# Optimization experiments

Measured on AMD Instinct MI355X. Metric: run time of the kernel, lower is better.

Reference implementation:

```python
import jax, jax.numpy as jnp
import numpy as np

TEMPERATURE = 0.1
EPS = 1e-8  # torch F.cosine_similarity denom clamp


def setup_inputs() -> dict:
    key = jax.random.key(0)
    k1, k2, k3 = jax.random.split(key, 3)
    B, M, D, K = 8, 256, 768, 100
    N = B * M
    transformer_outputs = jax.random.normal(k1, (B, M, D), dtype=jnp.float32)
    cnn_targets = jax.random.normal(k2, (B, M, D), dtype=jnp.float32)
    # uniform sampling with replacement over [0, N) excluding self (multinomial on uniform mask)
    r = jax.random.randint(k3, (N, K), 0, N - 1)
    i = jnp.arange(N)[:, None]
    neg_indices = (r + (r >= i)).astype(jnp.int32)
    return {"transformer_outputs": transformer_outputs, "cnn_targets": cnn_targets, "neg_indices": neg_indices}


def reference(transformer_outputs, cnn_targets, neg_indices):
    B, M, D = transformer_outputs.shape
    N = B * M
    preds = transformer_outputs.reshape(N, D)
    targets = cnn_targets.reshape(N, D)
    pn = preds / jnp.clip(jnp.linalg.norm(preds, axis=-1, keepdims=True), EPS)
    tn = targets / jnp.clip(jnp.linalg.norm(targets, axis=-1, keepdims=True), EPS)
    # all pairwise cosine sims [N, N]; positive on the diagonal, negatives gathered by index
    sim = pn @ tn.T
    pos = jnp.diagonal(sim)                                   # [N]
    neg = sim[jnp.arange(N)[:, None], neg_indices]            # [N, K]
    logits = jnp.concatenate([pos[:, None], neg], axis=1) / TEMPERATURE
    # cross-entropy with label 0 for every row
    loss = -jnp.mean(jax.nn.log_softmax(logits, axis=-1)[:, 0])
    return loss
```

## Files before the change

kernel.cpp:

```cpp
#include <hip/hip_runtime.h>
#include <hip/hip_bf16.h>
#include <math.h>

#define NROWS 2048
#define DDIM  768
#define KNEG  100
#define NLOGITS 101
#define MT 7
#define KW 6

typedef __attribute__((ext_vector_type(4))) float floatx4;

static constexpr float TEMP_INV = 10.0f;
static constexpr float EPS_NORM = 1e-8f;

__device__ __forceinline__ unsigned pack_fp8x4(float a, float b, float c, float d) {
    int u = 0;
    u = __builtin_amdgcn_cvt_pk_fp8_f32(a, b, u, false);
    u = __builtin_amdgcn_cvt_pk_fp8_f32(c, d, u, true);
    return (unsigned)u;
}

__global__ __launch_bounds__(256) void cl_prep_kernel(
        const float* __restrict__ targets,
        unsigned char* __restrict__ tn8) {
    const int wave = threadIdx.x >> 6, lane = threadIdx.x & 63;
    const int row = blockIdx.x * 4 + wave;
    const float4* tv = (const float4*)(targets + (size_t)row * DDIM);
    const float4 a0 = tv[2 * lane], a1 = tv[2 * lane + 1], b0 = tv[128 + lane];

    float ss = 0.f;
    ss = fmaf(a0.x, a0.x, ss); ss = fmaf(a0.y, a0.y, ss);
    ss = fmaf(a0.z, a0.z, ss); ss = fmaf(a0.w, a0.w, ss);
    ss = fmaf(a1.x, a1.x, ss); ss = fmaf(a1.y, a1.y, ss);
    ss = fmaf(a1.z, a1.z, ss); ss = fmaf(a1.w, a1.w, ss);
    ss = fmaf(b0.x, b0.x, ss); ss = fmaf(b0.y, b0.y, ss);
    ss = fmaf(b0.z, b0.z, ss); ss = fmaf(b0.w, b0.w, ss);
    #pragma unroll
    for (int off = 32; off > 0; off >>= 1) ss += __shfl_xor(ss, off);
    const float it = 1.0f / fmaxf(sqrtf(ss), EPS_NORM);

    const unsigned u0 = pack_fp8x4(a0.x * it, a0.y * it, a0.z * it, a0.w * it);
    const unsigned u1 = pack_fp8x4(a1.x * it, a1.y * it, a1.z * it, a1.w * it);
    const unsigned u2 = pack_fp8x4(b0.x * it, b0.y * it, b0.z * it, b0.w * it);

    __shared__ __align__(16) unsigned char buf[4][DDIM];
    *(uint2*)(&buf[wave][8 * lane]) = make_uint2(u0, u1);
    *(unsigned*)(&buf[wave][512 + 4 * lane]) = u2;
    __syncthreads();
    if (lane < 48)
        ((uint4*)(tn8 + (size_t)row * DDIM))[lane] = *(const uint4*)(&buf[wave][16 * lane]);
}

__global__ __launch_bounds__(256, 4) void cl_rowloss_kernel(
        const float* __restrict__ preds,
        const unsigned char* __restrict__ tn8,
        const int* __restrict__ neg_idx,
        float* __restrict__ row_loss) {
    const int i = blockIdx.x;
    const int tid = threadIdx.x;
    const int wave = tid >> 6, lane = tid & 63;

    __shared__ __align__(16) unsigned char Ab[2][16 * DDIM];
    __shared__ __align__(16) unsigned char pn8[DDIM];
    __shared__ __align__(16) float parts[4][MT * 16];
    __shared__ int idx_lds[MT * 16];

    if (tid < MT * 16)
        idx_lds[tid] = (tid == 0 || tid > KNEG) ? i : neg_idx[(size_t)i * KNEG + tid - 1];
    __syncthreads();

    auto stage = [&](int t, int buf) {
        #pragma unroll
        for (int it = 0; it < 3; ++it) {
            const int g = wave * 192 + it * 64 + lane;
            const int r = g / 48, c = g - r * 48;
            const unsigned char* src = tn8 + (size_t)idx_lds[t * 16 + r] * DDIM
                                       + ((c ^ (r & 7)) << 4);
            __builtin_amdgcn_global_load_lds(
                (const __attribute__((address_space(1))) void*)src,
                (__attribute__((address_space(3))) void*)&Ab[buf][(wave * 192 + it * 64) << 4],
                16, 0, 0);
        }
    };

    stage(0, 0);

    if (wave == 0) {
        const float4* pv = (const float4*)(preds + (size_t)i * DDIM);
        const float4 a0 = pv[2 * lane], a1 = pv[2 * lane + 1], b0 = pv[128 + lane];
        float ss = 0.f;
        ss = fmaf(a0.x, a0.x, ss); ss = fmaf(a0.y, a0.y, ss);
        ss = fmaf(a0.z, a0.z, ss); ss = fmaf(a0.w, a0.w, ss);
        ss = fmaf(a1.x, a1.x, ss); ss = fmaf(a1.y, a1.y, ss);
        ss = fmaf(a1.z, a1.z, ss); ss = fmaf(a1.w, a1.w, ss);
        ss = fmaf(b0.x, b0.x, ss); ss = fmaf(b0.y, b0.y, ss);
        ss = fmaf(b0.z, b0.z, ss); ss = fmaf(b0.w, b0.w, ss);
        #pragma unroll
        for (int off = 32; off > 0; off >>= 1) ss += __shfl_xor(ss, off);
        const float inv = 1.0f / fmaxf(sqrtf(ss), EPS_NORM);
        *(uint2*)(&pn8[8 * lane]) = make_uint2(
            pack_fp8x4(a0.x * inv, a0.y * inv, a0.z * inv, a0.w * inv),
            pack_fp8x4(a1.x * inv, a1.y * inv, a1.z * inv, a1.w * inv));
        *(unsigned*)(&pn8[512 + 4 * lane]) =
            pack_fp8x4(b0.x * inv, b0.y * inv, b0.z * inv, b0.w * inv);
    }
    __syncthreads();

    const int kb = wave * KW;
    const int q = lane >> 4;
    long long bfr[KW];
    #pragma unroll
    for (int kk = 0; kk < KW; ++kk)
        bfr[kk] = *(const long long*)(&pn8[(kb + kk) * 32 + q * 8]);

    const int aoff = (lane & 15) * DDIM + kb * 32 + q * 8;
    const int axor = (lane & 7) << 4;

    floatx4 acc[MT] = {};
    #pragma unroll
    for (int t = 0; t < MT; ++t) {
        if (t < MT - 1) stage(t + 1, (t + 1) & 1);
        const int cur = t & 1;
        #pragma unroll
        for (int kk = 0; kk < KW; ++kk) {
            const long long af = *(const long long*)(&Ab[cur][(aoff + kk * 32) ^ axor]);
            acc[t] = __builtin_amdgcn_mfma_f32_16x16x32_fp8_fp8(af, bfr[kk],
                                                                acc[t], 0, 0, 0);
        }
        __syncthreads();
    }

    if ((lane & 15) == 0) {
        const int rb = q * 4;
        #pragma unroll
        for (int t = 0; t < MT; ++t)
            *(floatx4*)(&parts[wave][t * 16 + rb]) = acc[t];
    }
    __syncthreads();

    if (wave == 0) {
        const float v0 = (parts[0][lane] + parts[1][lane] +
                          parts[2][lane] + parts[3][lane]) * TEMP_INV;
        float v1 = -INFINITY;
        if (lane <= NLOGITS - 65)
            v1 = (parts[0][64 + lane] + parts[1][64 + lane] +
                  parts[2][64 + lane] + parts[3][64 + lane]) * TEMP_INV;
        const float l0 = __shfl(v0, 0);
        float m = fmaxf(v0, v1);
        #pragma unroll
        for (int off = 32; off > 0; off >>= 1) m = fmaxf(m, __shfl_xor(m, off));
        float e = expf(v0 - m);
        if (lane <= NLOGITS - 65) e += expf(v1 - m);
        #pragma unroll
        for (int off = 32; off > 0; off >>= 1) e += __shfl_xor(e, off);
        if (lane == 0) row_loss[i] = (m + logf(e)) - l0;
    }
}

__global__ void cl_reduce_kernel(const float* __restrict__ row_loss,
                                 float* __restrict__ out) {
    const int tid = threadIdx.x;
    float s = 0.f;
    #pragma unroll
    for (int c = 0; c < 2; ++c) {
        const float4 v = ((const float4*)row_loss)[tid + 256 * c];
        s += (v.x + v.y) + (v.z + v.w);
    }
    #pragma unroll
    for (int off = 32; off > 0; off >>= 1) s += __shfl_down(s, off);
    __shared__ float sw[4];
    const int wave = tid >> 6, lane = tid & 63;
    if (lane == 0) sw[wave] = s;
    __syncthreads();
    if (tid == 0) out[0] = (sw[0] + sw[1] + sw[2] + sw[3]) / (float)NROWS;
}

extern "C" void kernel_launch(void* const* d_in, const int* in_sizes, int n_in,
                              void* d_out, int out_size, void* d_ws, size_t ws_size,
                              hipStream_t stream) {
    const float* preds   = (const float*)d_in[0];
    const float* targets = (const float*)d_in[1];
    const int*   neg_idx = (const int*)d_in[2];
    float* out = (float*)d_out;

    unsigned char* tn8 = (unsigned char*)d_ws;
    float* row_loss = (float*)((char*)d_ws + (size_t)NROWS * DDIM);

    cl_prep_kernel<<<NROWS / 4, 256, 0, stream>>>(targets, tn8);
    cl_rowloss_kernel<<<NROWS, 256, 0, stream>>>(preds, tn8, neg_idx, row_loss);
    cl_reduce_kernel<<<1, 256, 0, stream>>>(row_loss, out);
}
```

Measured before the change: 24.94 us.

## Triple-buffer gathered target tiles with explicit vmcnt waits and barriers

Switches the row-loss kernel's gathered-target staging from double to triple buffering, so two tiles are in flight ahead of the MFMA consumer. Full __syncthreads are replaced by partial s_waitcnt vmcnt plus raw s_barrier, so a wave only waits for the oldest tile's async LDS loads. The preds row load is also issued before the staging so its latency overlaps. This raises LDS use per block, which may reduce occupancy, and it depends on exact vmcnt counting being correct.

```diff
diff --git a/kernel.cpp b/kernel.cpp
--- a/kernel.cpp
+++ b/kernel.cpp
@@ -61,7 +61,7 @@
     const int tid = threadIdx.x;
     const int wave = tid >> 6, lane = tid & 63;
 
-    __shared__ __align__(16) unsigned char Ab[2][16 * DDIM];
+    __shared__ __align__(16) unsigned char Ab[3][16 * DDIM];
     __shared__ __align__(16) unsigned char pn8[DDIM];
     __shared__ __align__(16) float parts[4][MT * 16];
     __shared__ int idx_lds[MT * 16];
@@ -84,11 +84,16 @@
         }
     };
 
-    stage(0, 0);
-
+    float4 a0, a1, b0;
     if (wave == 0) {
         const float4* pv = (const float4*)(preds + (size_t)i * DDIM);
-        const float4 a0 = pv[2 * lane], a1 = pv[2 * lane + 1], b0 = pv[128 + lane];
+        a0 = pv[2 * lane]; a1 = pv[2 * lane + 1]; b0 = pv[128 + lane];
+    }
+
+    stage(0, 0);
+    stage(1, 1);
+
+    if (wave == 0) {
         float ss = 0.f;
         ss = fmaf(a0.x, a0.x, ss); ss = fmaf(a0.y, a0.y, ss);
         ss = fmaf(a0.z, a0.z, ss); ss = fmaf(a0.w, a0.w, ss);
@@ -105,7 +110,9 @@
         *(unsigned*)(&pn8[512 + 4 * lane]) =
             pack_fp8x4(b0.x * inv, b0.y * inv, b0.z * inv, b0.w * inv);
     }
-    __syncthreads();
+    asm volatile("s_waitcnt lgkmcnt(0)" ::: "memory");
+    __builtin_amdgcn_s_barrier();
+    __builtin_amdgcn_sched_barrier(0);
 
     const int kb = wave * KW;
     const int q = lane >> 4;
@@ -118,18 +125,33 @@
     const int axor = (lane & 7) << 4;
 
     floatx4 acc[MT] = {};
-    #pragma unroll
-    for (int t = 0; t < MT; ++t) {
-        if (t < MT - 1) stage(t + 1, (t + 1) & 1);
-        const int cur = t & 1;
-        #pragma unroll
-        for (int kk = 0; kk < KW; ++kk) {
-            const long long af = *(const long long*)(&Ab[cur][(aoff + kk * 32) ^ axor]);
-            acc[t] = __builtin_amdgcn_mfma_f32_16x16x32_fp8_fp8(af, bfr[kk],
-                                                                acc[t], 0, 0, 0);
-        }
-        __syncthreads();
-    }
+
+#define CL_ITER(T, NWAIT)                                                     \
+    {                                                                         \
+        if ((T) + 2 < MT) stage((T) + 2, ((T) + 2) % 3);                      \
+        asm volatile("s_waitcnt vmcnt(" #NWAIT ")" ::: "memory");             \
+        __builtin_amdgcn_s_barrier();                                         \
+        __builtin_amdgcn_sched_barrier(0);                                    \
+        _Pragma("unroll")                                                     \
+        for (int kk = 0; kk < KW; ++kk) {                                     \
+            const long long af =                                              \
+                *(const long long*)(&Ab[(T) % 3][(aoff + kk * 32) ^ axor]);   \
+            acc[T] = __builtin_amdgcn_mfma_f32_16x16x32_fp8_fp8(af, bfr[kk],  \
+                                                                acc[T], 0, 0, 0); \
+        }                                                                     \
+        asm volatile("s_waitcnt lgkmcnt(0)" ::: "memory");                    \
+        __builtin_amdgcn_s_barrier();                                         \
+        __builtin_amdgcn_sched_barrier(0);                                    \
+    }
+
+    CL_ITER(0, 6)
+    CL_ITER(1, 6)
+    CL_ITER(2, 6)
+    CL_ITER(3, 6)
+    CL_ITER(4, 6)
+    CL_ITER(5, 3)
+    CL_ITER(6, 0)
+#undef CL_ITER
 
     if ((lane & 15) == 0) {
         const int rb = q * 4;
```

Measured after the change: 25.32 us. Within noise of the previous version (+1.5%).
